# Kernel tuning notes

Hardware: AMD Instinct MI355X
Metric: run time of the kernel (lower is better)

The kernel has to match this reference:

```python
import jax, jax.numpy as jnp
import numpy as np

N = 50000
E = 800000
F_IN = 128
H = 128
M = 256


def setup_inputs() -> dict:
    key = jax.random.key(0)
    ks = jax.random.split(key, 12)
    x = jax.random.normal(ks[0], (N, F_IN), dtype=jnp.float32)
    edge_index = jax.random.randint(ks[1], (2, E), 0, N, dtype=jnp.int64)

    def glorot(k, shape):
        fan_in, fan_out = shape
        s = jnp.sqrt(6.0 / (fan_in + fan_out)).astype(jnp.float32)
        return jax.random.uniform(k, shape, jnp.float32, -s, s)

    return {
        "x": x,
        "edge_index": edge_index,
        # SAGEConv1: lin_l (neighbor aggregate, with bias), lin_r (root, no bias)
        "W1l": glorot(ks[2], (F_IN, H)), "b1l": jnp.zeros((H,), jnp.float32),
        "W1r": glorot(ks[3], (F_IN, H)),
        # SAGEConv2
        "W2l": glorot(ks[4], (H, H)), "b2l": jnp.zeros((H,), jnp.float32),
        "W2r": glorot(ks[5], (H, H)),
        # edge MLP: Linear(2H -> M), ReLU, Linear(M -> 1)
        "W3": glorot(ks[6], (2 * H, M)), "b3": jnp.zeros((M,), jnp.float32),
        "W4": glorot(ks[7], (M, 1)), "b4": jnp.zeros((1,), jnp.float32),
    }


def _sage_conv(x, src, dst, Wl, bl, Wr, num_nodes):
    # mean aggregation of source-node features at destination nodes
    agg = jax.ops.segment_sum(x[src], dst, num_segments=num_nodes)  # [N, F]
    cnt = jax.ops.segment_sum(jnp.ones((src.shape[0],), x.dtype), dst,
                              num_segments=num_nodes)
    agg = agg / jnp.maximum(cnt, 1.0)[:, None]
    # out = lin_l(agg) + lin_r(x)
    return agg @ Wl + bl + x @ Wr


def reference(x, edge_index, W1l, b1l, W1r, W2l, b2l, W2r, W3, b3, W4, b4):
    src, dst = edge_index[0], edge_index[1]
    h = jax.nn.relu(_sage_conv(x, src, dst, W1l, b1l, W1r, N))   # dropout: eval mode, identity
    h = jax.nn.relu(_sage_conv(h, src, dst, W2l, b2l, W2r, N))
    edge_feat = jnp.concatenate([h[src], h[dst]], axis=-1)       # [E, 2H]
    hidden = jax.nn.relu(edge_feat @ W3 + b3)                    # [E, M]
    pred = hidden @ W4 + b4                                      # [E, 1]
    return pred.reshape(-1)
```

## Files before the change

kernel.cpp:

```cpp
#include <hip/hip_runtime.h>
#include <hip/hip_bf16.h>

#define NN 50000
#define NE 800000
#define SCAN_G ((NN + 255) / 256)

typedef __attribute__((ext_vector_type(8))) short short8;
typedef __attribute__((ext_vector_type(4))) float f32x4;

__device__ inline float bf_lo(unsigned u) { u <<= 16; float f; __builtin_memcpy(&f, &u, 4); return f; }
__device__ inline float bf_hi(unsigned u) { u &= 0xffff0000u; float f; __builtin_memcpy(&f, &u, 4); return f; }
__device__ inline unsigned pack_bf16x2(float a, float b) {
    __hip_bfloat16 ba = __float2bfloat16(a), bb = __float2bfloat16(b);
    unsigned short ua, ub;
    __builtin_memcpy(&ua, &ba, 2);
    __builtin_memcpy(&ub, &bb, 2);
    return (unsigned)ua | ((unsigned)ub << 16);
}
__device__ inline __hip_bfloat16 f2bf(float a) { return __float2bfloat16(a); }

__global__ void prep_wpq(const float* __restrict__ W3, __hip_bfloat16* __restrict__ wpq) {
    const int idx4 = (blockIdx.x * 256 + threadIdx.x) * 4;
    const int c = idx4 >> 7;
    const int k0 = idx4 & 127;
#pragma unroll
    for (int i = 0; i < 4; ++i) {
        const int k = k0 + i;
        const float v = (c < 256) ? W3[k * 256 + c] : W3[(128 + k) * 256 + (c - 256)];
        wpq[c * 128 + k] = __float2bfloat16(v);
    }
}

__global__ void prep_w12t(const float* __restrict__ W1l, const float* __restrict__ W1r,
                          const float* __restrict__ W2l, const float* __restrict__ W2r,
                          __hip_bfloat16* __restrict__ w12t) {
    const int idx = blockIdx.x * 256 + threadIdx.x;
    const int layer = idx >> 15;
    const int c = (idx >> 7) & 255;
    const int k = idx & 127;
    const float* W = layer ? (c < 128 ? W2l : W2r) : (c < 128 ? W1l : W1r);
    w12t[idx] = __float2bfloat16(W[k * 128 + (c & 127)]);
}

__global__ __launch_bounds__(256) void hist_kernel(const int* __restrict__ ei,
                                                   int* __restrict__ cnt) {
    for (int e = blockIdx.x * 256 + threadIdx.x; e < NE; e += gridDim.x * 256)
        atomicAdd(&cnt[ei[NE + e]], 1);
}

__global__ __launch_bounds__(256) void scan_blk(const int* __restrict__ cnt,
                                                int* __restrict__ off,
                                                int* __restrict__ bsum) {
    __shared__ int sm[256];
    const int t = threadIdx.x;
    const int i = blockIdx.x * 256 + t;
    const int v = (i < NN) ? cnt[i] : 0;
    sm[t] = v;
    __syncthreads();
    for (int d = 1; d < 256; d <<= 1) {
        const int add = (t >= d) ? sm[t - d] : 0;
        __syncthreads();
        sm[t] += add;
        __syncthreads();
    }
    if (i < NN) off[i] = sm[t] - v;
    if (t == 255) bsum[blockIdx.x] = sm[255];
}

__global__ __launch_bounds__(256) void scan_top(int* __restrict__ bsum) {
    __shared__ int sm[256];
    const int t = threadIdx.x;
    const int v = (t < SCAN_G) ? bsum[t] : 0;
    sm[t] = v;
    __syncthreads();
    for (int d = 1; d < 256; d <<= 1) {
        const int add = (t >= d) ? sm[t - d] : 0;
        __syncthreads();
        sm[t] += add;
        __syncthreads();
    }
    if (t < SCAN_G) bsum[t] = sm[t] - v;
}

__global__ __launch_bounds__(256) void scan_add(int* __restrict__ off,
                                                int* __restrict__ cursor,
                                                const int* __restrict__ bsum) {
    const int t = threadIdx.x;
    const int i = blockIdx.x * 256 + t;
    if (i < NN) {
        const int v = off[i] + bsum[blockIdx.x];
        off[i] = v;
        cursor[i] = v;
    }
    if (i == NN - 1) off[NN] = NE;
}

__global__ __launch_bounds__(256) void fill_kernel(const int* __restrict__ ei,
                                                   int* __restrict__ cursor,
                                                   int* __restrict__ ssrc,
                                                   int* __restrict__ sdst,
                                                   int* __restrict__ seid) {
    for (int e = blockIdx.x * 256 + threadIdx.x; e < NE; e += gridDim.x * 256) {
        const int d = ei[NE + e];
        const int p = atomicAdd(&cursor[d], 1);
        ssrc[p] = ei[e];
        sdst[p] = d;
        seid[p] = e;
    }
}

template <bool IN_F32>
__global__ __launch_bounds__(256) void proj_gemm(const void* __restrict__ inp,
                                                 const __hip_bfloat16* __restrict__ wt,
                                                 __hip_bfloat16* __restrict__ ob) {
    __shared__ __align__(16) char A[16384];
    const int t = threadIdx.x;
    const int n0 = blockIdx.x * 64;
    {
        const int row = t >> 2, part = t & 3;
        const int node = n0 + row;
        const int sw = (row & 7) << 4;
        if (IN_F32) {
            const float* xp = (const float*)inp + (size_t)node * 128 + part * 32;
#pragma unroll
            for (int i = 0; i < 8; ++i) {
                uint2 w = make_uint2(0u, 0u);
                if (node < NN) {
                    const float4 v = *(const float4*)(xp + i * 4);
                    w.x = pack_bf16x2(v.x, v.y);
                    w.y = pack_bf16x2(v.z, v.w);
                }
                const int inner = part * 64 + i * 8;
                *(uint2*)(A + row * 256 + (inner ^ sw)) = w;
            }
        } else {
            const char* srcp = (const char*)((const __hip_bfloat16*)inp + (size_t)node * 128);
#pragma unroll
            for (int i = 0; i < 4; ++i) {
                const int inner = part * 64 + i * 16;
                uint4 v = make_uint4(0u, 0u, 0u, 0u);
                if (node < NN) v = *(const uint4*)(srcp + inner);
                *(uint4*)(A + row * 256 + (inner ^ sw)) = v;
            }
        }
    }
    __syncthreads();

    const int w = t >> 6, l = t & 63;
    const int lr = l & 15, lg = l >> 4;
    const int cb = w * 64;
    f32x4 acc[4][4] = {};
    for (int ks = 0; ks < 4; ++ks) {
        short8 af[4], bf[4];
        const int innerA = ks * 64 + lg * 16;
#pragma unroll
        for (int rt = 0; rt < 4; ++rt) {
            const int row = rt * 16 + lr;
            af[rt] = *(const short8*)(A + row * 256 + (innerA ^ ((row & 7) << 4)));
        }
        const int kidx = ks * 32 + lg * 8;
#pragma unroll
        for (int ct = 0; ct < 4; ++ct) {
            const int col = cb + ct * 16 + lr;
            bf[ct] = *(const short8*)(wt + col * 128 + kidx);
        }
#pragma unroll
        for (int rt = 0; rt < 4; ++rt)
#pragma unroll
            for (int ct = 0; ct < 4; ++ct)
                acc[rt][ct] = __builtin_amdgcn_mfma_f32_16x16x32_bf16(af[rt], bf[ct], acc[rt][ct], 0, 0, 0);
    }
#pragma unroll
    for (int rt = 0; rt < 4; ++rt) {
        __syncthreads();
#pragma unroll
        for (int ct = 0; ct < 4; ++ct) {
            const int col = cb + ct * 16 + lr;
#pragma unroll
            for (int j = 0; j < 4; ++j) {
                const int row = lg * 4 + j;
                *(__hip_bfloat16*)(A + row * 528 + col * 2) = f2bf(acc[rt][ct][j]);
            }
        }
        __syncthreads();
        const int row = t >> 4, cc = t & 15;
        const int node = n0 + rt * 16 + row;
        if (node < NN) {
#pragma unroll
            for (int pass = 0; pass < 2; ++pass) {
                const int byteoff = pass * 256 + cc * 16;
                *(uint4*)((char*)(ob + (size_t)node * 256) + byteoff) =
                    *(const uint4*)(A + row * 528 + byteoff);
            }
        }
    }
}

__global__ __launch_bounds__(256) void gather_fuse(const __hip_bfloat16* __restrict__ ob,
                                                   const int* __restrict__ off,
                                                   const int* __restrict__ ssrc,
                                                   const float* __restrict__ bl,
                                                   __hip_bfloat16* __restrict__ outp) {
    const int wv = threadIdx.x >> 6, lane = threadIdx.x & 63;
    const float2 bv = *(const float2*)&bl[lane * 2];
    for (int n = blockIdx.x * 4 + wv; n < NN; n += gridDim.x * 4) {
        const int b = off[n], e = off[n + 1];
        float a0 = 0.f, a1 = 0.f;
        int i = b;
        int s0 = (i + 0 < e) ? ssrc[i + 0] : 0;
        int s1 = (i + 1 < e) ? ssrc[i + 1] : 0;
        int s2 = (i + 2 < e) ? ssrc[i + 2] : 0;
        int s3 = (i + 3 < e) ? ssrc[i + 3] : 0;
        for (; i + 4 <= e;) {
            const unsigned u0 = *(const unsigned*)(ob + (size_t)s0 * 256 + lane * 2);
            const unsigned u1 = *(const unsigned*)(ob + (size_t)s1 * 256 + lane * 2);
            const unsigned u2 = *(const unsigned*)(ob + (size_t)s2 * 256 + lane * 2);
            const unsigned u3 = *(const unsigned*)(ob + (size_t)s3 * 256 + lane * 2);
            i += 4;
            s0 = (i + 0 < e) ? ssrc[i + 0] : 0;
            s1 = (i + 1 < e) ? ssrc[i + 1] : 0;
            s2 = (i + 2 < e) ? ssrc[i + 2] : 0;
            s3 = (i + 3 < e) ? ssrc[i + 3] : 0;
            a0 += bf_lo(u0) + bf_lo(u1) + bf_lo(u2) + bf_lo(u3);
            a1 += bf_hi(u0) + bf_hi(u1) + bf_hi(u2) + bf_hi(u3);
        }
        if (i < e) {
            const unsigned u = *(const unsigned*)(ob + (size_t)s0 * 256 + lane * 2);
            a0 += bf_lo(u); a1 += bf_hi(u); ++i;
            if (i < e) {
                const unsigned u1_ = *(const unsigned*)(ob + (size_t)s1 * 256 + lane * 2);
                a0 += bf_lo(u1_); a1 += bf_hi(u1_); ++i;
                if (i < e) {
                    const unsigned u2_ = *(const unsigned*)(ob + (size_t)s2 * 256 + lane * 2);
                    a0 += bf_lo(u2_); a1 += bf_hi(u2_);
                }
            }
        }
        const float inv = 1.0f / fmaxf((float)(e - b), 1.0f);
        const unsigned uz = *(const unsigned*)(ob + (size_t)n * 256 + 128 + lane * 2);
        const float h0 = fmaxf(a0 * inv + bf_lo(uz) + bv.x, 0.0f);
        const float h1 = fmaxf(a1 * inv + bf_hi(uz) + bv.y, 0.0f);
        *(unsigned*)((char*)outp + (size_t)n * 256 + lane * 4) = pack_bf16x2(h0, h1);
    }
}

__global__ __launch_bounds__(256) void pq_gemm(const __hip_bfloat16* __restrict__ h2b,
                                               const __hip_bfloat16* __restrict__ wpq,
                                               const float* __restrict__ b3,
                                               __hip_bfloat16* __restrict__ pqb) {
    __shared__ __align__(16) char A[16640];
    const int t = threadIdx.x;
    const int n0 = blockIdx.x * 64;
    {
        const int row = t >> 2, part = t & 3;
        const int node = n0 + row;
        const int sw = (row & 7) << 4;
#pragma unroll
        for (int i = 0; i < 4; ++i) {
            const int inner = part * 64 + i * 16;
            uint4 v = make_uint4(0u, 0u, 0u, 0u);
            if (node < NN) v = *(const uint4*)((const char*)(h2b + node * 128) + inner);
            *(uint4*)(A + row * 256 + (inner ^ sw)) = v;
        }
    }
    __syncthreads();

    const int w = t >> 6, l = t & 63;
    const int lr = l & 15, lg = l >> 4;
    const int cb = w * 128;
    f32x4 acc[4][8] = {};
    for (int ks = 0; ks < 4; ++ks) {
        short8 af[4], bf[8];
        const int innerA = ks * 64 + lg * 16;
#pragma unroll
        for (int rt = 0; rt < 4; ++rt) {
            const int row = rt * 16 + lr;
            af[rt] = *(const short8*)(A + row * 256 + (innerA ^ ((row & 7) << 4)));
        }
        const int kidx = ks * 32 + lg * 8;
#pragma unroll
        for (int ct = 0; ct < 8; ++ct) {
            const int col = cb + ct * 16 + lr;
            bf[ct] = *(const short8*)(wpq + col * 128 + kidx);
        }
#pragma unroll
        for (int rt = 0; rt < 4; ++rt)
#pragma unroll
            for (int ct = 0; ct < 8; ++ct)
                acc[rt][ct] = __builtin_amdgcn_mfma_f32_16x16x32_bf16(af[rt], bf[ct], acc[rt][ct], 0, 0, 0);
    }
    float badd[8];
#pragma unroll
    for (int ct = 0; ct < 8; ++ct) {
        const int col = cb + ct * 16 + lr;
        badd[ct] = (col >= 256) ? b3[col - 256] : 0.f;
    }
#pragma unroll
    for (int rt = 0; rt < 4; ++rt) {
        __syncthreads();
#pragma unroll
        for (int ct = 0; ct < 8; ++ct) {
            const int col = cb + ct * 16 + lr;
#pragma unroll
            for (int j = 0; j < 4; ++j) {
                const int row = lg * 4 + j;
                *(__hip_bfloat16*)(A + row * 1040 + col * 2) = f2bf(acc[rt][ct][j] + badd[ct]);
            }
        }
        __syncthreads();
        const int row = t >> 4, cc = t & 15;
        const int node = n0 + rt * 16 + row;
        if (node < NN) {
#pragma unroll
            for (int pass = 0; pass < 4; ++pass) {
                const int byteoff = pass * 256 + cc * 16;
                *(uint4*)((char*)(pqb + (size_t)node * 512) + byteoff) =
                    *(const uint4*)(A + row * 1040 + byteoff);
            }
        }
    }
}

__global__ __launch_bounds__(256) void edge_kernel(const int* __restrict__ ssrc,
                                                   const int* __restrict__ sdst,
                                                   const int* __restrict__ seid,
                                                   const __hip_bfloat16* __restrict__ pqb,
                                                   const float* __restrict__ W4,
                                                   const float* __restrict__ b4,
                                                   float* __restrict__ out) {
    const int i = threadIdx.x & 7;
    const int g = threadIdx.x >> 3;
    float w4r[4][8];
#pragma unroll
    for (int j = 0; j < 4; ++j)
#pragma unroll
        for (int u = 0; u < 8; ++u)
            w4r[j][u] = W4[i * 8 + j * 64 + u];
    const float b4v = b4[0];
    for (int p = blockIdx.x * 32 + g; p < NE; p += gridDim.x * 32) {
        const int s = ssrc[p], d = sdst[p], eid = seid[p];
        const char* Pp = (const char*)(pqb + (size_t)s * 512 + i * 8);
        const char* Qp = (const char*)(pqb + (size_t)d * 512 + 256 + i * 8);
        float acc = 0.f;
#pragma unroll
        for (int j = 0; j < 4; ++j) {
            const uint4 pv = *(const uint4*)(Pp + j * 128);
            const uint4 qv = *(const uint4*)(Qp + j * 128);
            const unsigned pa[4] = {pv.x, pv.y, pv.z, pv.w};
            const unsigned qa[4] = {qv.x, qv.y, qv.z, qv.w};
#pragma unroll
            for (int q4 = 0; q4 < 4; ++q4) {
                const float hlo = fmaxf(bf_lo(pa[q4]) + bf_lo(qa[q4]), 0.f);
                const float hhi = fmaxf(bf_hi(pa[q4]) + bf_hi(qa[q4]), 0.f);
                acc = fmaf(hlo, w4r[j][q4 * 2], acc);
                acc = fmaf(hhi, w4r[j][q4 * 2 + 1], acc);
            }
        }
        acc += __shfl_xor(acc, 1);
        acc += __shfl_xor(acc, 2);
        acc += __shfl_xor(acc, 4);
        if (i == 0) out[eid] = acc + b4v;
    }
}

extern "C" void kernel_launch(void* const* d_in, const int* in_sizes, int n_in,
                              void* d_out, int out_size, void* d_ws, size_t ws_size,
                              hipStream_t stream) {
    const float* x   = (const float*)d_in[0];
    const int* ei    = (const int*)d_in[1];
    const float* W1l = (const float*)d_in[2];
    const float* b1l = (const float*)d_in[3];
    const float* W1r = (const float*)d_in[4];
    const float* W2l = (const float*)d_in[5];
    const float* b2l = (const float*)d_in[6];
    const float* W2r = (const float*)d_in[7];
    const float* W3  = (const float*)d_in[8];
    const float* b3  = (const float*)d_in[9];
    const float* W4  = (const float*)d_in[10];
    const float* b4  = (const float*)d_in[11];
    float* out = (float*)d_out;

    char* ws = (char*)d_ws;
    int* cnt            = (int*)(ws);
    int* off            = (int*)(ws + 200704);
    int* cursor         = (int*)(ws + 401408);
    int* ssrc           = (int*)(ws + 602112);
    int* sdst           = (int*)(ws + 3802112);
    int* seid           = (int*)(ws + 7002112);
    __hip_bfloat16* pqb = (__hip_bfloat16*)(ws + 10202112);
    __hip_bfloat16* h1b = (__hip_bfloat16*)(ws + 23002112);
    __hip_bfloat16* ob  = (__hip_bfloat16*)(ws + 35802112);
    __hip_bfloat16* h2b = (__hip_bfloat16*)(ws + 61402112);
    __hip_bfloat16* wpq = (__hip_bfloat16*)(ws + 74202112);
    __hip_bfloat16* w12t= (__hip_bfloat16*)(ws + 74333184);

    hipMemsetAsync(cnt, 0, NN * sizeof(int), stream);
    hist_kernel<<<1024, 256, 0, stream>>>(ei, cnt);
    scan_blk<<<SCAN_G, 256, 0, stream>>>(cnt, off, cursor + NN);
    scan_top<<<1, 256, 0, stream>>>(cursor + NN);
    scan_add<<<SCAN_G, 256, 0, stream>>>(off, cursor, cursor + NN);
    fill_kernel<<<1024, 256, 0, stream>>>(ei, cursor, ssrc, sdst, seid);
    prep_wpq<<<64, 256, 0, stream>>>(W3, wpq);
    prep_w12t<<<256, 256, 0, stream>>>(W1l, W1r, W2l, W2r, w12t);

    proj_gemm<true><<<(NN + 63) / 64, 256, 0, stream>>>((const void*)x, w12t, ob);
    gather_fuse<<<2048, 256, 0, stream>>>(ob, off, ssrc, b1l, h1b);
    proj_gemm<false><<<(NN + 63) / 64, 256, 0, stream>>>((const void*)h1b, w12t + 256 * 128, ob);
    gather_fuse<<<2048, 256, 0, stream>>>(ob, off, ssrc, b2l, h2b);
    pq_gemm<<<(NN + 63) / 64, 256, 0, stream>>>(h2b, wpq, b3, pqb);
    edge_kernel<<<2048, 256, 0, stream>>>(ssrc, sdst, seid, pqb, W4, b4, out);
}
```

Baseline: 394.3 us.

## Pack dst/eid into int2, deepen gather prefetch, process two edges per group

```diff
diff --git a/kernel.cpp b/kernel.cpp
--- a/kernel.cpp
+++ b/kernel.cpp
@@ -98,14 +98,12 @@
 __global__ __launch_bounds__(256) void fill_kernel(const int* __restrict__ ei,
                                                    int* __restrict__ cursor,
                                                    int* __restrict__ ssrc,
-                                                   int* __restrict__ sdst,
-                                                   int* __restrict__ seid) {
+                                                   int2* __restrict__ sde) {
     for (int e = blockIdx.x * 256 + threadIdx.x; e < NE; e += gridDim.x * 256) {
         const int d = ei[NE + e];
         const int p = atomicAdd(&cursor[d], 1);
         ssrc[p] = ei[e];
-        sdst[p] = d;
-        seid[p] = e;
+        sde[p] = make_int2(d, e);
     }
 }
 
@@ -206,35 +204,24 @@
     for (int n = blockIdx.x * 4 + wv; n < NN; n += gridDim.x * 4) {
         const int b = off[n], e = off[n + 1];
         float a0 = 0.f, a1 = 0.f;
+        int idx[8];
+#pragma unroll
+        for (int k = 0; k < 8; ++k) idx[k] = (b + k < e) ? ssrc[b + k] : 0;
         int i = b;
-        int s0 = (i + 0 < e) ? ssrc[i + 0] : 0;
-        int s1 = (i + 1 < e) ? ssrc[i + 1] : 0;
-        int s2 = (i + 2 < e) ? ssrc[i + 2] : 0;
-        int s3 = (i + 3 < e) ? ssrc[i + 3] : 0;
-        for (; i + 4 <= e;) {
-            const unsigned u0 = *(const unsigned*)(ob + (size_t)s0 * 256 + lane * 2);
-            const unsigned u1 = *(const unsigned*)(ob + (size_t)s1 * 256 + lane * 2);
-            const unsigned u2 = *(const unsigned*)(ob + (size_t)s2 * 256 + lane * 2);
-            const unsigned u3 = *(const unsigned*)(ob + (size_t)s3 * 256 + lane * 2);
-            i += 4;
-            s0 = (i + 0 < e) ? ssrc[i + 0] : 0;
-            s1 = (i + 1 < e) ? ssrc[i + 1] : 0;
-            s2 = (i + 2 < e) ? ssrc[i + 2] : 0;
-            s3 = (i + 3 < e) ? ssrc[i + 3] : 0;
-            a0 += bf_lo(u0) + bf_lo(u1) + bf_lo(u2) + bf_lo(u3);
-            a1 += bf_hi(u0) + bf_hi(u1) + bf_hi(u2) + bf_hi(u3);
-        }
-        if (i < e) {
-            const unsigned u = *(const unsigned*)(ob + (size_t)s0 * 256 + lane * 2);
-            a0 += bf_lo(u); a1 += bf_hi(u); ++i;
-            if (i < e) {
-                const unsigned u1_ = *(const unsigned*)(ob + (size_t)s1 * 256 + lane * 2);
-                a0 += bf_lo(u1_); a1 += bf_hi(u1_); ++i;
-                if (i < e) {
-                    const unsigned u2_ = *(const unsigned*)(ob + (size_t)s2 * 256 + lane * 2);
-                    a0 += bf_lo(u2_); a1 += bf_hi(u2_);
-                }
-            }
+        for (; i + 8 <= e;) {
+            unsigned u[8];
+#pragma unroll
+            for (int k = 0; k < 8; ++k)
+                u[k] = *(const unsigned*)(ob + (size_t)idx[k] * 256 + lane * 2);
+            i += 8;
+#pragma unroll
+            for (int k = 0; k < 8; ++k) idx[k] = (i + k < e) ? ssrc[i + k] : 0;
+#pragma unroll
+            for (int k = 0; k < 8; ++k) { a0 += bf_lo(u[k]); a1 += bf_hi(u[k]); }
+        }
+        for (int k = 0; i < e; ++i, ++k) {
+            const unsigned u = *(const unsigned*)(ob + (size_t)idx[k] * 256 + lane * 2);
+            a0 += bf_lo(u); a1 += bf_hi(u);
         }
         const float inv = 1.0f / fmaxf((float)(e - b), 1.0f);
         const unsigned uz = *(const unsigned*)(ob + (size_t)n * 256 + 128 + lane * 2);
@@ -322,8 +309,7 @@
 }
 
 __global__ __launch_bounds__(256) void edge_kernel(const int* __restrict__ ssrc,
-                                                   const int* __restrict__ sdst,
-                                                   const int* __restrict__ seid,
+                                                   const int2* __restrict__ sde,
                                                    const __hip_bfloat16* __restrict__ pqb,
                                                    const float* __restrict__ W4,
                                                    const float* __restrict__ b4,
@@ -337,29 +323,49 @@
         for (int u = 0; u < 8; ++u)
             w4r[j][u] = W4[i * 8 + j * 64 + u];
     const float b4v = b4[0];
-    for (int p = blockIdx.x * 32 + g; p < NE; p += gridDim.x * 32) {
-        const int s = ssrc[p], d = sdst[p], eid = seid[p];
-        const char* Pp = (const char*)(pqb + (size_t)s * 512 + i * 8);
-        const char* Qp = (const char*)(pqb + (size_t)d * 512 + 256 + i * 8);
-        float acc = 0.f;
+    for (int p = blockIdx.x * 64 + g * 2; p < NE; p += gridDim.x * 64) {
+        const int s0 = ssrc[p], s1 = ssrc[p + 1];
+        const int2 de0 = sde[p], de1 = sde[p + 1];
+        const char* P0 = (const char*)(pqb + (size_t)s0 * 512 + i * 8);
+        const char* Q0 = (const char*)(pqb + (size_t)de0.x * 512 + 256 + i * 8);
+        const char* P1 = (const char*)(pqb + (size_t)s1 * 512 + i * 8);
+        const char* Q1 = (const char*)(pqb + (size_t)de1.x * 512 + 256 + i * 8);
+        uint4 pv0[4], qv0[4], pv1[4], qv1[4];
 #pragma unroll
         for (int j = 0; j < 4; ++j) {
-            const uint4 pv = *(const uint4*)(Pp + j * 128);
-            const uint4 qv = *(const uint4*)(Qp + j * 128);
-            const unsigned pa[4] = {pv.x, pv.y, pv.z, pv.w};
-            const unsigned qa[4] = {qv.x, qv.y, qv.z, qv.w};
+            pv0[j] = *(const uint4*)(P0 + j * 128);
+            qv0[j] = *(const uint4*)(Q0 + j * 128);
+            pv1[j] = *(const uint4*)(P1 + j * 128);
+            qv1[j] = *(const uint4*)(Q1 + j * 128);
+        }
+        float acc0 = 0.f, acc1 = 0.f;
+#pragma unroll
+        for (int j = 0; j < 4; ++j) {
+            const unsigned pa0[4] = {pv0[j].x, pv0[j].y, pv0[j].z, pv0[j].w};
+            const unsigned qa0[4] = {qv0[j].x, qv0[j].y, qv0[j].z, qv0[j].w};
+            const unsigned pa1[4] = {pv1[j].x, pv1[j].y, pv1[j].z, pv1[j].w};
+            const unsigned qa1[4] = {qv1[j].x, qv1[j].y, qv1[j].z, qv1[j].w};
 #pragma unroll
             for (int q4 = 0; q4 < 4; ++q4) {
-                const float hlo = fmaxf(bf_lo(pa[q4]) + bf_lo(qa[q4]), 0.f);
-                const float hhi = fmaxf(bf_hi(pa[q4]) + bf_hi(qa[q4]), 0.f);
-                acc = fmaf(hlo, w4r[j][q4 * 2], acc);
-                acc = fmaf(hhi, w4r[j][q4 * 2 + 1], acc);
-            }
-        }
-        acc += __shfl_xor(acc, 1);
-        acc += __shfl_xor(acc, 2);
-        acc += __shfl_xor(acc, 4);
-        if (i == 0) out[eid] = acc + b4v;
+                const float h0l = fmaxf(bf_lo(pa0[q4]) + bf_lo(qa0[q4]), 0.f);
+                const float h0h = fmaxf(bf_hi(pa0[q4]) + bf_hi(qa0[q4]), 0.f);
+                acc0 = fmaf(h0l, w4r[j][q4 * 2], acc0);
+                acc0 = fmaf(h0h, w4r[j][q4 * 2 + 1], acc0);
+                const float h1l = fmaxf(bf_lo(pa1[q4]) + bf_lo(qa1[q4]), 0.f);
+                const float h1h = fmaxf(bf_hi(pa1[q4]) + bf_hi(qa1[q4]), 0.f);
+                acc1 = fmaf(h1l, w4r[j][q4 * 2], acc1);
+                acc1 = fmaf(h1h, w4r[j][q4 * 2 + 1], acc1);
+            }
+        }
+#pragma unroll
+        for (int m = 1; m <= 4; m <<= 1) {
+            acc0 += __shfl_xor(acc0, m);
+            acc1 += __shfl_xor(acc1, m);
+        }
+        if (i == 0) {
+            out[de0.y] = acc0 + b4v;
+            out[de1.y] = acc1 + b4v;
+        }
     }
 }
 
@@ -385,8 +391,7 @@
     int* off            = (int*)(ws + 200704);
     int* cursor         = (int*)(ws + 401408);
     int* ssrc           = (int*)(ws + 602112);
-    int* sdst           = (int*)(ws + 3802112);
-    int* seid           = (int*)(ws + 7002112);
+    int2* sde           = (int2*)(ws + 3802112);
     __hip_bfloat16* pqb = (__hip_bfloat16*)(ws + 10202112);
     __hip_bfloat16* h1b = (__hip_bfloat16*)(ws + 23002112);
     __hip_bfloat16* ob  = (__hip_bfloat16*)(ws + 35802112);
@@ -399,7 +404,7 @@
     scan_blk<<<SCAN_G, 256, 0, stream>>>(cnt, off, cursor + NN);
     scan_top<<<1, 256, 0, stream>>>(cursor + NN);
     scan_add<<<SCAN_G, 256, 0, stream>>>(off, cursor, cursor + NN);
-    fill_kernel<<<1024, 256, 0, stream>>>(ei, cursor, ssrc, sdst, seid);
+    fill_kernel<<<1024, 256, 0, stream>>>(ei, cursor, ssrc, sde);
     prep_wpq<<<64, 256, 0, stream>>>(W3, wpq);
     prep_w12t<<<256, 256, 0, stream>>>(W1l, W1r, W2l, W2r, w12t);
 
@@ -408,5 +413,5 @@
     proj_gemm<false><<<(NN + 63) / 64, 256, 0, stream>>>((const void*)h1b, w12t + 256 * 128, ob);
     gather_fuse<<<2048, 256, 0, stream>>>(ob, off, ssrc, b2l, h2b);
     pq_gemm<<<(NN + 63) / 64, 256, 0, stream>>>(h2b, wpq, b3, pqb);
-    edge_kernel<<<2048, 256, 0, stream>>>(ssrc, sdst, seid, pqb, W4, b4, out);
-}
+    edge_kernel<<<2048, 256, 0, stream>>>(ssrc, sde, pqb, W4, b4, out);
+}
```

Result: slower. 405.6 us (+2.9%).
